# Kernel tuning notes

Measured on AMD Instinct MI355X. Metric: run time of the kernel, lower is better.

## Reference

```python
import jax, jax.numpy as jnp
import numpy as np

L, E, H, FFE = 4, 512, 8, 512  # layers, embed, heads, ff dim (must equal E for residual)
HD = E // H


def _ln(x, g, b):
    mu = jnp.mean(x, -1, keepdims=True)
    var = jnp.mean((x - mu) ** 2, -1, keepdims=True)
    return (x - mu) / jnp.sqrt(var + 1e-5) * g + b


def setup_inputs() -> dict:
    key = jax.random.key(0)
    ks = jax.random.split(key, 8)
    B, S = 8, 128
    w = lambda k, shape: jax.random.normal(k, shape, jnp.float32) * 0.02
    return {
        "x": jax.random.normal(ks[0], (B, S, E), jnp.float32),
        "Wq": w(ks[1], (L, E, E)), "bq": jnp.zeros((L, E), jnp.float32),
        "Wk": w(ks[2], (L, E, E)), "bk": jnp.zeros((L, E), jnp.float32),
        "Wv": w(ks[3], (L, E, E)), "bv": jnp.zeros((L, E), jnp.float32),
        "Wo": w(ks[4], (L, E, E)), "bo": jnp.zeros((L, E), jnp.float32),
        "Wf": w(ks[5], (L, E, FFE)), "bf": jnp.zeros((L, FFE), jnp.float32),
        "g1": jnp.ones((L, E), jnp.float32), "b1": jnp.zeros((L, E), jnp.float32),
        "g2": jnp.ones((L, FFE), jnp.float32), "b2": jnp.zeros((L, FFE), jnp.float32),
    }


def reference(x, Wq, bq, Wk, bk, Wv, bv, Wo, bo, Wf, bf, g1, b1, g2, b2):
    B, S, _ = x.shape

    def stack(xb, mask):
        # xb: [B,S,E]; mask: [S] bool, True = key position inside current prefix.
        # Non-causal MHA restricted to prefix keys exactly reproduces running
        # the original stack on x[:, :s, :] (query positions beyond the prefix
        # produce values we never read).
        h = xb
        for l in range(L):
            q = (h @ Wq[l] + bq[l]).reshape(B, S, H, HD)
            k = (h @ Wk[l] + bk[l]).reshape(B, S, H, HD)
            v = (h @ Wv[l] + bv[l]).reshape(B, S, H, HD)
            sc = jnp.einsum('bqhd,bkhd->bhqk', q, k) / jnp.sqrt(jnp.float32(HD))
            sc = jnp.where(mask[None, None, None, :], sc, jnp.float32(-1e9))
            a = jax.nn.softmax(sc, axis=-1)
            o = jnp.einsum('bhqk,bkhd->bqhd', a, v).reshape(B, S, E)
            h = _ln(o @ Wo[l] + bo[l] + h, g1[l], b1[l])          # MHA + residual + LN1
            h = _ln(jax.nn.relu(h @ Wf[l] + bf[l]) + h, g2[l], b2[l])  # FF + ReLU + residual + LN2
        return h

    # masks[s-1] selects keys 0..s-1 -> prefix of length s
    masks = jnp.tril(jnp.ones((S, S), bool))
    outs = jax.vmap(stack, in_axes=(None, 0))(x, masks)  # [S, B, S, E]
    idx = jnp.arange(S)
    last = outs[idx, :, idx]  # [S, B, E]: last valid token of each prefix run
    return jnp.transpose(last, (1, 0, 2))  # [B, S, E]
```

## Files before the change

### kernel.cpp

```cpp
#include <hip/hip_runtime.h>
#include <stdint.h>

typedef unsigned short u16;
typedef __attribute__((ext_vector_type(8))) short bf16x8;
typedef __attribute__((ext_vector_type(4))) float f32x4;

#define EE 512
#define NH 8
#define HDm 64
#define SS 128
#define NB 8
#define NL 4
#define QKVW 1536

__device__ __forceinline__ float bf2f(u16 v){ union{uint32_t u; float f;} c; c.u=((uint32_t)v)<<16; return c.f; }
__device__ __forceinline__ u16 f2bf(float f){ union{float f; uint32_t u;} c; c.f=f; uint32_t u=c.u; return (u16)((u + 0x7FFFu + ((u>>16)&1u))>>16); }

__device__ __forceinline__ f32x4 mfma16(bf16x8 a, bf16x8 b, f32x4 c){
  return __builtin_amdgcn_mfma_f32_16x16x32_bf16(a,b,c,0,0,0);
}

__device__ __forceinline__ void gload16(const u16* g, u16* l){
  auto gp = reinterpret_cast<const __attribute__((address_space(1))) uint32_t*>(reinterpret_cast<uintptr_t>(g));
  auto lp = reinterpret_cast<__attribute__((address_space(3))) uint32_t*>(reinterpret_cast<uintptr_t>(l));
  __builtin_amdgcn_global_load_lds(gp, lp, 16, 0, 0);
}

#define ABAR() asm volatile("s_barrier" ::: "memory")
#define SB0()  __builtin_amdgcn_sched_barrier(0)
#define PRIO1() __builtin_amdgcn_s_setprio(1)
#define PRIO0() __builtin_amdgcn_s_setprio(0)

__device__ __forceinline__ void run_map(int bid, int cb, int U, int& r, int& u){
  int rr = 0;
  for (;;){
    int g = (cb + rr) >> 4;
    int gend = ((g + 1) << 4) - cb;
    int upr = (g + 1) * U;
    int span = (gend - rr) * upr;
    if (bid < span){ r = rr + bid / upr; u = bid % upr; return; }
    bid -= span; rr = gend;
  }
}
__device__ __forceinline__ void run_map256(int bid, int cb, int& r, int& u){
  int rr = 0;
  for (;;){
    int g = (cb + rr) >> 5;
    int gend = ((g + 1) << 5) - cb;
    int upr = g + 1;
    int span = (gend - rr) * upr;
    if (bid < span){ r = rr + bid / upr; u = bid % upr; return; }
    bid -= span; rr = gend;
  }
}

__global__ __launch_bounds__(256) void wtransT(const float* __restrict__ W, u16* __restrict__ dst,
                                               int dstL, int dstOff){
  __shared__ float tl[32][33];
  int l = blockIdx.y;
  int tile = blockIdx.x;
  int ot = tile & 15, it = tile >> 4;
  int t = threadIdx.x;
  int c = t & 31, r = t >> 5;
  #pragma unroll
  for (int k=0;k<4;k++){
    int ri = it*32 + r + k*8;
    tl[c][r + k*8] = W[(size_t)l*262144 + (size_t)ri*512 + ot*32 + c];
  }
  __syncthreads();
  #pragma unroll
  for (int k=0;k<4;k++){
    int ro = ot*32 + r + k*8;
    dst[(size_t)l*dstL + (size_t)(dstOff + ro)*512 + it*32 + c] = f2bf(tl[r + k*8][c]);
  }
}

__global__ __launch_bounds__(256) void bfuse(const float* __restrict__ bq, const float* __restrict__ bk,
                                             const float* __restrict__ bv, float* __restrict__ bqkv){
  int i = blockIdx.x*256 + threadIdx.x;
  int l = i / QKVW, n = i % QKVW;
  const float* b = (n < 512) ? bq : ((n < 1024) ? bk : bv);
  bqkv[i] = b[l*EE + (n & 511)];
}

__global__ __launch_bounds__(256) void hinit(const float* __restrict__ x, u16* __restrict__ h0){
  int i = (blockIdx.x*256 + threadIdx.x)*8;
  int e = i & 511;
  int pb = i >> 9;
  int b = pb & 7, pp = pb >> 3;
  const float* xp = x + (((size_t)b*SS + pp)<<9) + e;
  union{ bf16x8 v; u16 u[8]; } r;
  #pragma unroll
  for (int j=0;j<8;j++) r.u[j] = f2bf(xp[j]);
  *(bf16x8*)(h0 + i) = r.v;
}

template<int MODE>
__global__ __launch_bounds__(512, 2) void gemm256(const u16* __restrict__ A, const u16* __restrict__ Bt,
                                                  const float* __restrict__ bias,
                                                  const u16* __restrict__ res, size_t res_mask,
                                                  u16* __restrict__ o0, u16* __restrict__ o1, u16* __restrict__ o2,
                                                  int cb){
  extern __shared__ u16 lds[];
  int t = threadIdx.x;
  size_t m0;
  if (cb < 0){
    m0 = (size_t)blockIdx.x * 256;
  } else {
    int r, tile; run_map256(blockIdx.x, cb, r, tile);
    m0 = (size_t)r*1024 + (size_t)tile*256;
  }
  int n0 = blockIdx.y * 256;
  int wid = t>>6, lane = t&63;
  int wm = wid>>2, wn = wid&3;
  int lr = lane&15, lq = lane>>4;

  auto stage = [&](int kt, int h){
    int slot = (2*kt + h) & 3;
    u16* sb = lds + slot*16384;
    int k0 = kt*64;
    #pragma unroll
    for (int j=0;j<2;j++){
      int ch = j*512 + t;
      int row = ch>>3, cg = (ch&7) ^ (row&7);
      gload16(A  + (m0 + (size_t)(h*128 + row))*EE + k0 + cg*8, sb + ch*8);
      gload16(Bt + (size_t)(n0 + h*128 + row)*EE   + k0 + cg*8, sb + 8192 + ch*8);
    }
  };
  auto rdA = [&](int kt, int mi, int kk)->bf16x8{
    int slot = (2*kt + wm) & 3;
    int row = mi*16 + lr;
    int c = (kk*4 + lq) ^ (row&7);
    return *(const bf16x8*)(lds + slot*16384 + row*64 + c*8);
  };
  auto rdB = [&](int kt, int ni, int kk)->bf16x8{
    int slot = (2*kt + (wn>>1)) & 3;
    int row = (wn&1)*64 + ni*16 + lr;
    int c = (kk*4 + lq) ^ (row&7);
    return *(const bf16x8*)(lds + slot*16384 + 8192 + row*64 + c*8);
  };

  f32x4 acc[8][4] = {};
  stage(0,0); stage(0,1); stage(1,0); stage(1,1);

  #pragma unroll
  for (int kt=0; kt<8; kt++){
    if (kt < 7) asm volatile("s_waitcnt vmcnt(8)" ::: "memory");
    else        asm volatile("s_waitcnt vmcnt(0)" ::: "memory");
    ABAR();
    bf16x8 b0[4][2], a[4][2];
    #pragma unroll
    for (int ni=0;ni<4;ni++){ b0[ni][0]=rdB(kt,ni,0); b0[ni][1]=rdB(kt,ni,1); }
    #pragma unroll
    for (int mi=0;mi<4;mi++){ a[mi][0]=rdA(kt,mi,0); a[mi][1]=rdA(kt,mi,1); }
    PRIO1();
    #pragma unroll
    for (int mi=0;mi<4;mi++)
      #pragma unroll
      for (int ni=0;ni<2;ni++)
        #pragma unroll
        for (int kk=0;kk<2;kk++)
          acc[mi][ni] = mfma16(a[mi][kk], b0[ni][kk], acc[mi][ni]);
    PRIO0(); SB0(); ABAR();
    PRIO1();
    #pragma unroll
    for (int mi=0;mi<4;mi++)
      #pragma unroll
      for (int ni=2;ni<4;ni++)
        #pragma unroll
        for (int kk=0;kk<2;kk++)
          acc[mi][ni] = mfma16(a[mi][kk], b0[ni][kk], acc[mi][ni]);
    PRIO0(); SB0(); ABAR();
    #pragma unroll
    for (int mi=0;mi<4;mi++){ a[mi][0]=rdA(kt,mi+4,0); a[mi][1]=rdA(kt,mi+4,1); }
    PRIO1();
    #pragma unroll
    for (int mi=0;mi<4;mi++)
      #pragma unroll
      for (int ni=0;ni<2;ni++)
        #pragma unroll
        for (int kk=0;kk<2;kk++)
          acc[mi+4][ni] = mfma16(a[mi][kk], b0[ni][kk], acc[mi+4][ni]);
    PRIO0(); SB0(); ABAR();
    if (kt < 6){ stage(kt+2,0); stage(kt+2,1); }
    PRIO1();
    #pragma unroll
    for (int mi=0;mi<4;mi++)
      #pragma unroll
      for (int ni=2;ni<4;ni++)
        #pragma unroll
        for (int kk=0;kk<2;kk++)
          acc[mi+4][ni] = mfma16(a[mi][kk], b0[ni][kk], acc[mi+4][ni]);
    PRIO0(); SB0(); ABAR();
  }

  u16* outp;
  int nb;
  if (MODE==0){ int sel = n0 >> 9; outp = sel==0 ? o0 : (sel==1 ? o1 : o2); nb = n0 & 511; }
  else        { outp = o0; nb = n0; }
  #pragma unroll
  for (int ni=0;ni<4;ni++){
    int coln = wn*64 + ni*16 + lr;
    float bv = bias[n0 + coln];
    int col = nb + coln;
    #pragma unroll
    for (int mi=0;mi<8;mi++){
      #pragma unroll
      for (int j=0;j<4;j++){
        size_t row = m0 + (size_t)(wm*128 + mi*16 + lq*4 + j);
        float v = acc[mi][ni][j] + bv;
        if (MODE==2) v = fmaxf(v, 0.f);
        if (MODE>=1) v += bf2f(res[(row & res_mask)*EE + col]);
        outp[row*EE + col] = f2bf(v);
      }
    }
  }
}

__global__ __launch_bounds__(256) void attn(const u16* __restrict__ Q, const u16* __restrict__ K,
                                            const u16* __restrict__ V, u16* __restrict__ Oq,
                                            int cb, int shared_qkv){
  __shared__ u16 Ks[128*72];
  __shared__ u16 Vt[64*136];
  __shared__ u16 Ps[4][16*136];
  int t = threadIdx.x;
  int idx = blockIdx.x;
  int hh = idx & 7, b = (idx>>3)&7, r = idx>>6;
  int m_run = cb + r;
  const size_t RS = (size_t)SS*NB*EE;
  size_t rbase = shared_qkv ? 0 : (size_t)r*RS;
  size_t hb = (size_t)b*EE + hh*HDm;
  size_t obase = (size_t)r*RS + hb;
  int nkc = m_run/32 + 1;
  int nkt = nkc*2;
  int nqt = m_run/16 + 1;
  int nkr = nkt*16;
  for (int i=t; i<nkr*8; i+=256){
    int row=i>>3, c=(i&7)*8;
    *(uint4*)(Ks + row*72 + c) = *(const uint4*)(K + rbase + (size_t)row*NB*EE + hb + c);
  }
  for (int i=t; i<nkr*8; i+=256){
    int row=i>>3, c=(i&7)*8;
    uint4 raw = *(const uint4*)(V + rbase + (size_t)row*NB*EE + hb + c);
    const u16* pv = (const u16*)&raw;
    #pragma unroll
    for (int j=0;j<8;j++) Vt[(c+j)*136 + row] = pv[j];
  }
  __syncthreads();
  int wid=t>>6, lane=t&63, lr=lane&15, g=lane>>4, lk=(lane>>4)*8;
  u16* Pw = Ps[wid];
  for (int iq=0; iq<2; iq++){
    int qt = wid*2 + iq;
    if (qt >= nqt) continue;
    const u16* qrow = Q + rbase + (size_t)(qt*16+lr)*NB*EE + hb;
    bf16x8 qa0 = *(const bf16x8*)(qrow + lk);
    bf16x8 qa1 = *(const bf16x8*)(qrow + 32 + lk);
    f32x4 sc[8];
    #pragma unroll
    for (int kt=0;kt<8;kt++){
      if (kt < nkt){
        f32x4 c = {};
        bf16x8 kb0 = *(const bf16x8*)(Ks + (kt*16+lr)*72 + lk);
        bf16x8 kb1 = *(const bf16x8*)(Ks + (kt*16+lr)*72 + 32 + lk);
        c = mfma16(qa0, kb0, c);
        c = mfma16(qa1, kb1, c);
        int key = kt*16 + lr;
        #pragma unroll
        for (int i2=0;i2<4;i2++)
          sc[kt][i2] = (key <= m_run) ? c[i2]*0.125f : -1e9f;
      }
    }
    #pragma unroll
    for (int i2=0;i2<4;i2++){
      float v = -3.0e38f;
      #pragma unroll
      for (int kt=0;kt<8;kt++) if (kt<nkt) v = fmaxf(v, sc[kt][i2]);
      v = fmaxf(v, __shfl_xor(v,1));
      v = fmaxf(v, __shfl_xor(v,2));
      v = fmaxf(v, __shfl_xor(v,4));
      v = fmaxf(v, __shfl_xor(v,8));
      float s = 0.f;
      #pragma unroll
      for (int kt=0;kt<8;kt++) if (kt<nkt){ float e2=__expf(sc[kt][i2]-v); sc[kt][i2]=e2; s+=e2; }
      s += __shfl_xor(s,1); s += __shfl_xor(s,2); s += __shfl_xor(s,4); s += __shfl_xor(s,8);
      float inv = 1.f/s;
      #pragma unroll
      for (int kt=0;kt<8;kt++) if (kt<nkt) sc[kt][i2] *= inv;
    }
    #pragma unroll
    for (int kt=0;kt<8;kt++) if (kt<nkt){
      #pragma unroll
      for (int i2=0;i2<4;i2++)
        Pw[(g*4+i2)*136 + kt*16 + lr] = f2bf(sc[kt][i2]);
    }
    f32x4 oa[4] = {};
    #pragma unroll
    for (int kc=0;kc<4;kc++) if (kc<nkc){
      bf16x8 pa = *(const bf16x8*)(Pw + lr*136 + kc*32 + lk);
      #pragma unroll
      for (int dt=0;dt<4;dt++){
        bf16x8 vb = *(const bf16x8*)(Vt + (dt*16+lr)*136 + kc*32 + lk);
        oa[dt] = mfma16(pa, vb, oa[dt]);
      }
    }
    #pragma unroll
    for (int dt=0;dt<4;dt++){
      #pragma unroll
      for (int j=0;j<4;j++){
        size_t prow = (size_t)(qt*16 + g*4 + j);
        Oq[obase + prow*NB*EE + dt*16 + lr] = f2bf(oa[dt][j]);
      }
    }
  }
}

__global__ __launch_bounds__(256) void lnorm(const u16* __restrict__ in, const float* __restrict__ gg,
                                             const float* __restrict__ bb, u16* __restrict__ outp, int cb){
  int r, u; run_map(blockIdx.x, cb, 32, r, u);
  size_t row = (size_t)r*1024 + (size_t)u*4 + (threadIdx.x>>6);
  int lane = threadIdx.x & 63;
  const u16* p = in + row*EE + lane*8;
  union{ bf16x8 v; u16 u[8]; } d; d.v = *(const bf16x8*)p;
  float f[8]; float s=0.f;
  #pragma unroll
  for (int j=0;j<8;j++){ f[j]=bf2f(d.u[j]); s+=f[j]; }
  #pragma unroll
  for (int o=1;o<64;o<<=1) s += __shfl_xor(s,o);
  float mu = s*(1.f/512.f);
  float s2=0.f;
  #pragma unroll
  for (int j=0;j<8;j++){ float tt=f[j]-mu; s2+=tt*tt; }
  #pragma unroll
  for (int o=1;o<64;o<<=1) s2 += __shfl_xor(s2,o);
  float rstd = rsqrtf(s2*(1.f/512.f)+1e-5f);
  union{ bf16x8 v; u16 u[8]; } rr;
  #pragma unroll
  for (int j=0;j<8;j++) rr.u[j] = f2bf((f[j]-mu)*rstd*gg[lane*8+j] + bb[lane*8+j]);
  *(bf16x8*)(outp + row*EE + lane*8) = rr.v;
}

__global__ __launch_bounds__(256) void extract(const u16* __restrict__ h, float* __restrict__ out, int cb){
  int i = blockIdx.x*256 + threadIdx.x;
  int e = i & 511;
  int b = (i >> 9) & 7;
  int r = i >> 12;
  int m = cb + r;
  out[((size_t)b*SS + m)*EE + e] = bf2f(h[(((size_t)r*SS + m)*NB + b)*EE + e]);
}

extern "C" void kernel_launch(void* const* d_in, const int* in_sizes, int n_in,
                              void* d_out, int out_size, void* d_ws, size_t ws_size,
                              hipStream_t stream){
  const float* x   = (const float*)d_in[0];
  const float* Wq  = (const float*)d_in[1];
  const float* bq  = (const float*)d_in[2];
  const float* Wk  = (const float*)d_in[3];
  const float* bk  = (const float*)d_in[4];
  const float* Wv  = (const float*)d_in[5];
  const float* bv  = (const float*)d_in[6];
  const float* Wo  = (const float*)d_in[7];
  const float* bo  = (const float*)d_in[8];
  const float* Wf  = (const float*)d_in[9];
  const float* bfb = (const float*)d_in[10];
  const float* g1  = (const float*)d_in[11];
  const float* b1  = (const float*)d_in[12];
  const float* g2  = (const float*)d_in[13];
  const float* b2  = (const float*)d_in[14];
  float* out = (float*)d_out;

  hipFuncSetAttribute((const void*)gemm256<0>, hipFuncAttributeMaxDynamicSharedMemorySize, 131072);
  hipFuncSetAttribute((const void*)gemm256<1>, hipFuncAttributeMaxDynamicSharedMemorySize, 131072);
  hipFuncSetAttribute((const void*)gemm256<2>, hipFuncAttributeMaxDynamicSharedMemorySize, 131072);

  uint8_t* p = (uint8_t*)d_ws;
  u16* WqkvT = (u16*)p; p += (size_t)NL*QKVW*EE*2;
  u16* WoT   = (u16*)p; p += (size_t)NL*EE*EE*2;
  u16* WfT   = (u16*)p; p += (size_t)NL*EE*EE*2;
  float* bqkv= (float*)p; p += (size_t)NL*QKVW*4;
  u16* h0    = (u16*)p; p += (size_t)SS*NB*EE*2;
  u16* q0    = (u16*)p; p += (size_t)SS*NB*EE*2;
  u16* k0    = (u16*)p; p += (size_t)SS*NB*EE*2;
  u16* v0    = (u16*)p; p += (size_t)SS*NB*EE*2;
  size_t used = (size_t)(p - (uint8_t*)d_ws);

  int RC = 128;
  const size_t PER_RUN = (size_t)SS*NB*EE*2*5;
  while (RC > 1 && used + (size_t)RC*PER_RUN > ws_size) RC >>= 1;

  const size_t BUF = (size_t)RC*SS*NB*EE*2;
  u16* h   = (u16*)p; p += BUF;
  u16* q   = (u16*)p; p += BUF;
  u16* k   = (u16*)p; p += BUF;
  u16* v   = (u16*)p; p += BUF;
  u16* tmp = (u16*)p; p += BUF;

  const size_t NOMASK = ~(size_t)0;
  const int QL = QKVW*EE;
  const int OL = EE*EE;

  wtransT<<<dim3(256,NL),256,0,stream>>>(Wq, WqkvT, QL, 0);
  wtransT<<<dim3(256,NL),256,0,stream>>>(Wk, WqkvT, QL, 512);
  wtransT<<<dim3(256,NL),256,0,stream>>>(Wv, WqkvT, QL, 1024);
  wtransT<<<dim3(256,NL),256,0,stream>>>(Wo, WoT, OL, 0);
  wtransT<<<dim3(256,NL),256,0,stream>>>(Wf, WfT, OL, 0);
  bfuse<<<24,256,0,stream>>>(bq, bk, bv, bqkv);
  hinit<<<256,256,0,stream>>>(x, h0);
  gemm256<0><<<dim3(4,6),512,131072,stream>>>(h0, WqkvT, bqkv, nullptr, 0, q0, k0, v0, -1);

  for (int cb=0; cb<SS; cb+=RC){
    int t128 = 0, t256 = 0;
    for (int r2=0;r2<RC;r2++){ t128 += (cb+r2)/16 + 1; t256 += (cb+r2)/32 + 1; }

    attn<<<dim3(RC*64),256,0,stream>>>(q0, k0, v0, q, cb, 1);
    gemm256<1><<<dim3(t256,2),512,131072,stream>>>(q, WoT, bo, h0, (size_t)1023, tmp, nullptr, nullptr, cb);
    lnorm<<<dim3(t128*32),256,0,stream>>>(tmp, g1, b1, h, cb);
    gemm256<2><<<dim3(t256,2),512,131072,stream>>>(h, WfT, bfb, h, NOMASK, tmp, nullptr, nullptr, cb);
    lnorm<<<dim3(t128*32),256,0,stream>>>(tmp, g2, b2, h, cb);

    for (int l=1;l<NL;l++){
      gemm256<0><<<dim3(t256,6),512,131072,stream>>>(h, WqkvT+(size_t)l*QL, bqkv+l*QKVW, nullptr, 0, q, k, v, cb);
      attn<<<dim3(RC*64),256,0,stream>>>(q, k, v, q, cb, 0);
      gemm256<1><<<dim3(t256,2),512,131072,stream>>>(q, WoT+(size_t)l*OL, bo+l*EE, h, NOMASK, tmp, nullptr, nullptr, cb);
      lnorm<<<dim3(t128*32),256,0,stream>>>(tmp, g1+l*EE, b1+l*EE, h, cb);
      gemm256<2><<<dim3(t256,2),512,131072,stream>>>(h, WfT+(size_t)l*OL, bfb+l*EE, h, NOMASK, tmp, nullptr, nullptr, cb);
      lnorm<<<dim3(t128*32),256,0,stream>>>(tmp, g2+l*EE, b2+l*EE, h, cb);
    }
    extract<<<dim3(RC*16),256,0,stream>>>(h, out, cb);
  }
}
```

Before: 2.176 ms.

## Fuse LayerNorm and output extraction into full-row Wo/FF GEMM epilogues

Replaces the Wo and FF GEMMs plus separate LayerNorm kernels with a GEMM whose tile covers 128 rows by the full 512 columns. Row statistics are reduced across waves through LDS, and normalized output is written directly. The last layer also scatters the final tokens to the output, which removes the extract kernel and the tmp buffer. This cuts launches and round-trips of intermediate activations to memory. In exchange it uses a single-pass variance formula and a different tiling and occupancy for these GEMMs. The in-place write to h while reading h as a residual appears safe because each block owns its rows.

Measured after the change: 3.156 ms. 45.1% more time.

```diff
diff --git a/kernel.cpp b/kernel.cpp
--- a/kernel.cpp
+++ b/kernel.cpp
@@ -95,10 +95,8 @@
   *(bf16x8*)(h0 + i) = r.v;
 }
 
-template<int MODE>
 __global__ __launch_bounds__(512, 2) void gemm256(const u16* __restrict__ A, const u16* __restrict__ Bt,
                                                   const float* __restrict__ bias,
-                                                  const u16* __restrict__ res, size_t res_mask,
                                                   u16* __restrict__ o0, u16* __restrict__ o1, u16* __restrict__ o2,
                                                   int cb){
   extern __shared__ u16 lds[];
@@ -194,10 +192,9 @@
     PRIO0(); SB0(); ABAR();
   }
 
-  u16* outp;
-  int nb;
-  if (MODE==0){ int sel = n0 >> 9; outp = sel==0 ? o0 : (sel==1 ? o1 : o2); nb = n0 & 511; }
-  else        { outp = o0; nb = n0; }
+  int sel = n0 >> 9;
+  u16* outp = sel==0 ? o0 : (sel==1 ? o1 : o2);
+  int nb = n0 & 511;
   #pragma unroll
   for (int ni=0;ni<4;ni++){
     int coln = wn*64 + ni*16 + lr;
@@ -208,10 +205,144 @@
       #pragma unroll
       for (int j=0;j<4;j++){
         size_t row = m0 + (size_t)(wm*128 + mi*16 + lq*4 + j);
-        float v = acc[mi][ni][j] + bv;
+        outp[row*EE + col] = f2bf(acc[mi][ni][j] + bv);
+      }
+    }
+  }
+}
+
+template<int MODE>
+__global__ __launch_bounds__(512) void gemm_ln(const u16* __restrict__ A, const u16* __restrict__ Bt,
+                                               const float* __restrict__ bias, const u16* __restrict__ res,
+                                               size_t res_mask, const float* __restrict__ lng,
+                                               const float* __restrict__ lnb, u16* __restrict__ outh,
+                                               float* __restrict__ fout, int last, int cb){
+  extern __shared__ u16 lds[];
+  int t = threadIdx.x;
+  int r, tile; run_map(blockIdx.x, cb, 1, r, tile);
+  int m_run = cb + r;
+  size_t m0 = (size_t)r*1024 + (size_t)tile*128;
+  int wid=t>>6, lane=t&63;
+  int wm=wid>>2, wn=wid&3, lr=lane&15, lq=lane>>4;
+
+  auto stage = [&](int kt, int slot){
+    u16* sb = lds + slot*20480;
+    int k0 = kt*32;
+    #pragma unroll
+    for (int j=0;j<5;j++){
+      int ch = j*512 + t;
+      int row = ch>>2, c = ch&3;
+      const u16* src;
+      if (j == 0) src = A  + (m0 + (size_t)row)*EE + k0 + c*8;
+      else        src = Bt + ((size_t)(row-128))*EE + k0 + c*8;
+      gload16(src, sb + ch*8);
+    }
+  };
+
+  f32x4 acc[4][8] = {};
+  stage(0,0); stage(1,1);
+
+  #pragma unroll
+  for (int kt=0; kt<16; kt++){
+    int slot = kt & 1;
+    if (kt < 15) asm volatile("s_waitcnt vmcnt(5)" ::: "memory");
+    else         asm volatile("s_waitcnt vmcnt(0)" ::: "memory");
+    ABAR();
+    bf16x8 a[4], b[8];
+    #pragma unroll
+    for (int mi=0;mi<4;mi++){
+      int row = wm*64 + mi*16 + lr;
+      a[mi] = *(const bf16x8*)(lds + slot*20480 + row*32 + lq*8);
+    }
+    #pragma unroll
+    for (int ni=0;ni<8;ni++){
+      int brow = wn*128 + ni*16 + lr;
+      b[ni] = *(const bf16x8*)(lds + slot*20480 + 4096 + brow*32 + lq*8);
+    }
+    asm volatile("s_waitcnt lgkmcnt(0)" ::: "memory");
+    SB0();
+    ABAR();
+    if (kt < 14) stage(kt+2, slot);
+    PRIO1();
+    #pragma unroll
+    for (int mi=0;mi<4;mi++)
+      #pragma unroll
+      for (int ni=0;ni<8;ni++)
+        acc[mi][ni] = mfma16(a[mi], b[ni], acc[mi][ni]);
+    PRIO0();
+  }
+
+  f32x4 psum[4] = {{0,0,0,0},{0,0,0,0},{0,0,0,0},{0,0,0,0}};
+  f32x4 psq[4]  = {{0,0,0,0},{0,0,0,0},{0,0,0,0},{0,0,0,0}};
+  #pragma unroll
+  for (int ni=0;ni<8;ni++){
+    int col = wn*128 + ni*16 + lr;
+    float bb = bias[col];
+    #pragma unroll
+    for (int mi=0;mi<4;mi++){
+      #pragma unroll
+      for (int j=0;j<4;j++){
+        size_t row = m0 + (size_t)(wm*64 + mi*16 + lq*4 + j);
+        float v = acc[mi][ni][j] + bb;
         if (MODE==2) v = fmaxf(v, 0.f);
-        if (MODE>=1) v += bf2f(res[(row & res_mask)*EE + col]);
-        outp[row*EE + col] = f2bf(v);
+        v += bf2f(res[(row & res_mask)*EE + col]);
+        acc[mi][ni][j] = v;
+        psum[mi][j] += v; psq[mi][j] += v*v;
+      }
+    }
+  }
+  #pragma unroll
+  for (int o=1;o<16;o<<=1){
+    #pragma unroll
+    for (int mi=0;mi<4;mi++)
+      #pragma unroll
+      for (int j=0;j<4;j++){
+        psum[mi][j] += __shfl_xor(psum[mi][j], o);
+        psq[mi][j]  += __shfl_xor(psq[mi][j], o);
+      }
+  }
+  float2* red = (float2*)lds;
+  __syncthreads();
+  if (lr == 0){
+    #pragma unroll
+    for (int mi=0;mi<4;mi++)
+      #pragma unroll
+      for (int j=0;j<4;j++)
+        red[(wm*64 + mi*16 + lq*4 + j)*4 + wn] = make_float2(psum[mi][j], psq[mi][j]);
+  }
+  __syncthreads();
+  float mean_[4][4], rstd_[4][4];
+  #pragma unroll
+  for (int mi=0;mi<4;mi++){
+    #pragma unroll
+    for (int j=0;j<4;j++){
+      int row128 = wm*64 + mi*16 + lq*4 + j;
+      float2 s0 = red[row128*4+0], s1 = red[row128*4+1], s2 = red[row128*4+2], s3 = red[row128*4+3];
+      float sm = s0.x + s1.x + s2.x + s3.x;
+      float sq = s0.y + s1.y + s2.y + s3.y;
+      float mu = sm * (1.f/512.f);
+      float var = sq * (1.f/512.f) - mu*mu;
+      mean_[mi][j] = mu;
+      rstd_[mi][j] = rsqrtf(var + 1e-5f);
+    }
+  }
+  #pragma unroll
+  for (int ni=0;ni<8;ni++){
+    int col = wn*128 + ni*16 + lr;
+    float gg = lng[col], bb2 = lnb[col];
+    #pragma unroll
+    for (int mi=0;mi<4;mi++){
+      #pragma unroll
+      for (int j=0;j<4;j++){
+        float vv = (acc[mi][ni][j] - mean_[mi][j]) * rstd_[mi][j] * gg + bb2;
+        u16 hb = f2bf(vv);
+        size_t row = m0 + (size_t)(wm*64 + mi*16 + lq*4 + j);
+        outh[row*EE + col] = hb;
+        if (last){
+          int row16 = tile*128 + wm*64 + mi*16 + lq*4 + j;
+          int p = row16 >> 3, b3 = row16 & 7;
+          if (p == m_run) fout[((size_t)b3*SS + p)*EE + col] = bf2f(hb);
+        }
       }
     }
   }
@@ -314,40 +445,6 @@
   }
 }
 
-__global__ __launch_bounds__(256) void lnorm(const u16* __restrict__ in, const float* __restrict__ gg,
-                                             const float* __restrict__ bb, u16* __restrict__ outp, int cb){
-  int r, u; run_map(blockIdx.x, cb, 32, r, u);
-  size_t row = (size_t)r*1024 + (size_t)u*4 + (threadIdx.x>>6);
-  int lane = threadIdx.x & 63;
-  const u16* p = in + row*EE + lane*8;
-  union{ bf16x8 v; u16 u[8]; } d; d.v = *(const bf16x8*)p;
-  float f[8]; float s=0.f;
-  #pragma unroll
-  for (int j=0;j<8;j++){ f[j]=bf2f(d.u[j]); s+=f[j]; }
-  #pragma unroll
-  for (int o=1;o<64;o<<=1) s += __shfl_xor(s,o);
-  float mu = s*(1.f/512.f);
-  float s2=0.f;
-  #pragma unroll
-  for (int j=0;j<8;j++){ float tt=f[j]-mu; s2+=tt*tt; }
-  #pragma unroll
-  for (int o=1;o<64;o<<=1) s2 += __shfl_xor(s2,o);
-  float rstd = rsqrtf(s2*(1.f/512.f)+1e-5f);
-  union{ bf16x8 v; u16 u[8]; } rr;
-  #pragma unroll
-  for (int j=0;j<8;j++) rr.u[j] = f2bf((f[j]-mu)*rstd*gg[lane*8+j] + bb[lane*8+j]);
-  *(bf16x8*)(outp + row*EE + lane*8) = rr.v;
-}
-
-__global__ __launch_bounds__(256) void extract(const u16* __restrict__ h, float* __restrict__ out, int cb){
-  int i = blockIdx.x*256 + threadIdx.x;
-  int e = i & 511;
-  int b = (i >> 9) & 7;
-  int r = i >> 12;
-  int m = cb + r;
-  out[((size_t)b*SS + m)*EE + e] = bf2f(h[(((size_t)r*SS + m)*NB + b)*EE + e]);
-}
-
 extern "C" void kernel_launch(void* const* d_in, const int* in_sizes, int n_in,
                               void* d_out, int out_size, void* d_ws, size_t ws_size,
                               hipStream_t stream){
@@ -368,9 +465,9 @@
   const float* b2  = (const float*)d_in[14];
   float* out = (float*)d_out;
 
-  hipFuncSetAttribute((const void*)gemm256<0>, hipFuncAttributeMaxDynamicSharedMemorySize, 131072);
-  hipFuncSetAttribute((const void*)gemm256<1>, hipFuncAttributeMaxDynamicSharedMemorySize, 131072);
-  hipFuncSetAttribute((const void*)gemm256<2>, hipFuncAttributeMaxDynamicSharedMemorySize, 131072);
+  hipFuncSetAttribute((const void*)gemm256,    hipFuncAttributeMaxDynamicSharedMemorySize, 131072);
+  hipFuncSetAttribute((const void*)gemm_ln<1>, hipFuncAttributeMaxDynamicSharedMemorySize, 81920);
+  hipFuncSetAttribute((const void*)gemm_ln<2>, hipFuncAttributeMaxDynamicSharedMemorySize, 81920);
 
   uint8_t* p = (uint8_t*)d_ws;
   u16* WqkvT = (u16*)p; p += (size_t)NL*QKVW*EE*2;
@@ -384,7 +481,7 @@
   size_t used = (size_t)(p - (uint8_t*)d_ws);
 
   int RC = 128;
-  const size_t PER_RUN = (size_t)SS*NB*EE*2*5;
+  const size_t PER_RUN = (size_t)SS*NB*EE*2*4;
   while (RC > 1 && used + (size_t)RC*PER_RUN > ws_size) RC >>= 1;
 
   const size_t BUF = (size_t)RC*SS*NB*EE*2;
@@ -392,7 +489,6 @@
   u16* q   = (u16*)p; p += BUF;
   u16* k   = (u16*)p; p += BUF;
   u16* v   = (u16*)p; p += BUF;
-  u16* tmp = (u16*)p; p += BUF;
 
   const size_t NOMASK = ~(size_t)0;
   const int QL = QKVW*EE;
@@ -405,26 +501,23 @@
   wtransT<<<dim3(256,NL),256,0,stream>>>(Wf, WfT, OL, 0);
   bfuse<<<24,256,0,stream>>>(bq, bk, bv, bqkv);
   hinit<<<256,256,0,stream>>>(x, h0);
-  gemm256<0><<<dim3(4,6),512,131072,stream>>>(h0, WqkvT, bqkv, nullptr, 0, q0, k0, v0, -1);
+  gemm256<<<dim3(4,6),512,131072,stream>>>(h0, WqkvT, bqkv, q0, k0, v0, -1);
 
   for (int cb=0; cb<SS; cb+=RC){
     int t128 = 0, t256 = 0;
     for (int r2=0;r2<RC;r2++){ t128 += (cb+r2)/16 + 1; t256 += (cb+r2)/32 + 1; }
 
     attn<<<dim3(RC*64),256,0,stream>>>(q0, k0, v0, q, cb, 1);
-    gemm256<1><<<dim3(t256,2),512,131072,stream>>>(q, WoT, bo, h0, (size_t)1023, tmp, nullptr, nullptr, cb);
-    lnorm<<<dim3(t128*32),256,0,stream>>>(tmp, g1, b1, h, cb);
-    gemm256<2><<<dim3(t256,2),512,131072,stream>>>(h, WfT, bfb, h, NOMASK, tmp, nullptr, nullptr, cb);
-    lnorm<<<dim3(t128*32),256,0,stream>>>(tmp, g2, b2, h, cb);
+    gemm_ln<1><<<dim3(t128),512,81920,stream>>>(q, WoT, bo, h0, (size_t)1023, g1, b1, h, out, 0, cb);
+    gemm_ln<2><<<dim3(t128),512,81920,stream>>>(h, WfT, bfb, h, NOMASK, g2, b2, h, out, 0, cb);
 
     for (int l=1;l<NL;l++){
-      gemm256<0><<<dim3(t256,6),512,131072,stream>>>(h, WqkvT+(size_t)l*QL, bqkv+l*QKVW, nullptr, 0, q, k, v, cb);
+      gemm256<<<dim3(t256,6),512,131072,stream>>>(h, WqkvT+(size_t)l*QL, bqkv+l*QKVW, q, k, v, cb);
       attn<<<dim3(RC*64),256,0,stream>>>(q, k, v, q, cb, 0);
-      gemm256<1><<<dim3(t256,2),512,131072,stream>>>(q, WoT+(size_t)l*OL, bo+l*EE, h, NOMASK, tmp, nullptr, nullptr, cb);
-      lnorm<<<dim3(t128*32),256,0,stream>>>(tmp, g1+l*EE, b1+l*EE, h, cb);
-      gemm256<2><<<dim3(t256,2),512,131072,stream>>>(h, WfT+(size_t)l*OL, bfb+l*EE, h, NOMASK, tmp, nullptr, nullptr, cb);
-      lnorm<<<dim3(t128*32),256,0,stream>>>(tmp, g2+l*EE, b2+l*EE, h, cb);
-    }
-    extract<<<dim3(RC*16),256,0,stream>>>(h, out, cb);
-  }
-}
+      gemm_ln<1><<<dim3(t128),512,81920,stream>>>(q, WoT+(size_t)l*OL, bo+l*EE, h, NOMASK,
+                                                  g1+l*EE, b1+l*EE, h, out, 0, cb);
+      gemm_ln<2><<<dim3(t128),512,81920,stream>>>(h, WfT+(size_t)l*OL, bfb+l*EE, h, NOMASK,
+                                                  g2+l*EE, b2+l*EE, h, out, (l==NL-1) ? 1 : 0, cb);
+    }
+  }
+}
```
